# Optimization experiments

Hardware: AMD Instinct MI355X
Metric: run time of the kernel (lower is better)

## Reference

```python
import jax, jax.numpy as jnp
import numpy as np

DIM_IN = 32
DIM_OUT = 32
DIM_X = 64   # dim_internal
DIM_NL = 32
EPS_Q = 1e-4      # eps in default Q
TOL = 1e-3        # pos_def_tol
D22_EPS = 1.0     # d22_epsilon


def _model_param(X, Y, B2, C2, D12, D22_L, D22_U, D21, gamma):
    """Faithful port of REN_IQC_gamma._update_model_param (QR_fun=None, dim_in==dim_out)."""
    g = gamma[0, 0]
    Q = -EPS_Q * jnp.eye(DIM_OUT)
    R = -2.0 * g * jnp.eye(DIM_IN)
    S = jnp.eye(DIM_OUT, DIM_IN)
    # D22 = base + sym + skew (dim_in == dim_out)
    D22 = (g + D22_EPS) * jnp.eye(DIM_OUT, DIM_IN) + D22_L.T @ D22_L + (D22_U - D22_U.T)
    SD = S @ D22
    R_cal = R + SD + SD.T + D22.T @ Q @ D22
    R_cal_inv = jnp.linalg.inv(R_cal)
    M = D22.T @ Q + S
    C2_cal = M @ C2                      # (dim_in, dim_x)
    D21_cal = M @ D21 - D12.T            # (dim_in, dim_nl)
    vec_r = jnp.concatenate([C2_cal.T, D21_cal.T, B2], axis=0)   # (2*dim_x+dim_nl, dim_in)
    psi_r = vec_r @ R_cal_inv @ vec_r.T
    vec_q = jnp.concatenate([C2.T, D21.T, jnp.zeros((DIM_X, DIM_OUT), X.dtype)], axis=0)
    psi_q = vec_q @ Q @ vec_q.T
    n = 2 * DIM_X + DIM_NL
    H = X.T @ X + TOL * jnp.eye(n) + psi_r - psi_q
    i1, i2 = DIM_X, DIM_X + DIM_NL
    H11 = H[:i1, :i1]
    H21 = H[i1:i2, :i1]
    H22 = H[i1:i2, i1:i2]
    H31 = H[i2:, :i1]
    H32 = H[i2:, i1:i2]
    H33 = H[i2:, i2:]
    E = 0.5 * (H11 + H33 + Y - Y.T)
    E_inv = jnp.linalg.inv(E)
    Lam = 0.5 * jnp.diag(H22)            # Lambda (dim_nl,)
    D11 = -jnp.tril(H22, k=-1)           # strictly lower triangular
    C1 = -H21
    Fm = H31
    B1 = H32
    return Fm, B1, E_inv, Lam, D11, C1, D22


def reference(u_in, x0, X, Y, B2, C2, D12, D22_L, D22_U, D21, gamma):
    # Parameters are constant across time steps, so the per-step recompute in the
    # torch code collapses to a single evaluation with identical math.
    Fm, B1, E_inv, Lam, D11, C1, D22 = _model_param(X, Y, B2, C2, D12, D22_L, D22_U, D21, gamma)
    B = u_in.shape[0]
    nl_idx = jnp.arange(DIM_NL)

    def step(x, u_t):                    # x: (B, DIM_X), u_t: (B, DIM_IN)
        a = x @ C1.T + u_t @ D12.T       # (B, DIM_NL), constant part of v

        def inner(w, i):                 # forward substitution over strictly-lower D11
            v = a[:, i] + w @ D11[i]     # (B,)
            w = w.at[:, i].set(jnp.tanh(v / Lam[i]))
            return w, None

        w, _ = jax.lax.scan(inner, jnp.zeros((B, DIM_NL), u_in.dtype), nl_idx)
        x_new = (x @ Fm.T + w @ B1.T + u_t @ B2.T) @ E_inv.T
        y_t = x_new @ C2.T + w @ D21.T + u_t @ D22.T
        return x_new, y_t

    u_time = jnp.swapaxes(u_in, 0, 1)    # (T, B, DIM_IN)
    _, ys = jax.lax.scan(step, x0[:, 0, :], u_time)
    return jnp.swapaxes(ys, 0, 1)        # (B, T, DIM_OUT)


def setup_inputs() -> dict:
    key = jax.random.key(0)
    ks = jax.random.split(key, 10)
    std = 0.5
    n = 2 * DIM_X + DIM_NL
    B, T = 2048, 256
    return {
        "u_in": jax.random.normal(ks[0], (B, T, DIM_IN), jnp.float32),
        "x0": jax.random.normal(ks[1], (B, 1, DIM_X), jnp.float32),
        "X": jax.random.normal(ks[2], (n, n), jnp.float32) * std,
        "Y": jax.random.normal(ks[3], (DIM_X, DIM_X), jnp.float32) * std,
        "B2": jax.random.normal(ks[4], (DIM_X, DIM_IN), jnp.float32) * std,
        "C2": jax.random.normal(ks[5], (DIM_OUT, DIM_X), jnp.float32) * std,
        "D12": jax.random.normal(ks[6], (DIM_NL, DIM_IN), jnp.float32) * std,
        "D22_L": jax.random.normal(ks[7], (DIM_IN, DIM_IN), jnp.float32) * std,
        "D22_U": jax.random.normal(ks[8], (DIM_OUT, DIM_IN), jnp.float32) * std,
        "D21": jnp.zeros((DIM_OUT, DIM_NL), jnp.float32),   # registered buffer, fixed zero
        "gamma": jax.random.normal(ks[9], (1, 1), jnp.float32) * 3.0,
    }
```

## Files before the change

kernel.cpp:

```cpp
#include <hip/hip_runtime.h>
#include <math.h>

#define EPS_Q 1e-4
#define TOLC  1e-3

#define OFF_D22   0
#define OFF_RINV  1024
#define OFF_VR    2048
#define OFF_T1    7168
#define OFF_H     12288
#define OFF_E     37888
#define OFF_EI    41984
#define OFF_TMP   46080
#define OFF_TMP2  50176
#define D_END     54272

__global__ __launch_bounds__(256, 1) void prep1(
    const float* __restrict__ B2, const float* __restrict__ C2,
    const float* __restrict__ D12, const float* __restrict__ L,
    const float* __restrict__ U, const float* __restrict__ D21,
    const float* __restrict__ gam, double* __restrict__ wsd)
{
  __shared__ double aug[32][65];
  __shared__ double sFac[32];
  __shared__ int sPiv;
  const int tid = threadIdx.x;
  const double g = (double)gam[0];
  double* D22d = wsd + OFF_D22;

  for (int idx = tid; idx < 1024; idx += 256) {
    int i = idx >> 5, j = idx & 31;
    double s = (i == j) ? (g + 1.0) : 0.0;
    for (int k = 0; k < 32; ++k) s += (double)L[k*32+i] * (double)L[k*32+j];
    s += (double)U[i*32+j] - (double)U[j*32+i];
    D22d[idx] = s;
  }
  __syncthreads();
  for (int idx = tid; idx < 1024; idx += 256) {
    int i = idx >> 5, j = idx & 31;
    double s = (i == j) ? (-2.0 * g) : 0.0;
    s += D22d[i*32+j] + D22d[j*32+i];
    double q = 0.0;
    for (int k = 0; k < 32; ++k) q += D22d[k*32+i] * D22d[k*32+j];
    aug[i][j] = s - EPS_Q * q;
    aug[i][32+j] = (i == j) ? 1.0 : 0.0;
  }
  __syncthreads();
  for (int k = 0; k < 32; ++k) {
    if (tid < 64) {
      float mv = -1.f; int mi = k;
      if (tid < 32 && tid >= k) { mv = (float)fabs(aug[tid][k]); mi = tid; }
      #pragma unroll
      for (int o = 32; o; o >>= 1) {
        float ov = __shfl_xor(mv, o); int oi = __shfl_xor(mi, o);
        if (ov > mv) { mv = ov; mi = oi; }
      }
      if (tid == 0) sPiv = mi;
    }
    __syncthreads();
    int p = sPiv;
    if (p != k) for (int c = tid; c < 64; c += 256) { double t1 = aug[k][c]; aug[k][c] = aug[p][c]; aug[p][c] = t1; }
    __syncthreads();
    double pinv = 1.0 / aug[k][k];
    if (tid < 32 && tid != k) sFac[tid] = aug[tid][k];
    __syncthreads();
    for (int c = tid; c < 64; c += 256) aug[k][c] *= pinv;
    __syncthreads();
    for (int idx = tid; idx < 2048; idx += 256) {
      int r = idx >> 6, c = idx & 63;
      if (r != k) aug[r][c] -= sFac[r] * aug[k][c];
    }
    __syncthreads();
  }
  double* Rinv = wsd + OFF_RINV;
  for (int idx = tid; idx < 1024; idx += 256) Rinv[idx] = aug[idx >> 5][32 + (idx & 31)];

  double* vr = wsd + OFF_VR;
  for (int idx = tid; idx < 64*32; idx += 256) {
    int p = idx >> 5, k = idx & 31;
    double q = 0.0;
    for (int m = 0; m < 32; ++m) q += D22d[m*32+k] * (double)C2[m*64+p];
    vr[p*32+k] = (double)C2[k*64+p] - EPS_Q * q;
  }
  for (int idx = tid; idx < 32*32; idx += 256) {
    int p = idx >> 5, k = idx & 31;
    double q = 0.0;
    for (int m = 0; m < 32; ++m) q += D22d[m*32+k] * (double)D21[m*32+p];
    vr[(64+p)*32+k] = (double)D21[k*32+p] - EPS_Q * q - (double)D12[p*32+k];
  }
  for (int idx = tid; idx < 64*32; idx += 256) {
    int p = idx >> 5, k = idx & 31;
    vr[(96+p)*32+k] = (double)B2[p*32+k];
  }
  __syncthreads();
  double* T1 = wsd + OFF_T1;
  for (int idx = tid; idx < 160*32; idx += 256) {
    int p = idx >> 5, k2 = idx & 31;
    double s = 0.0;
    for (int k = 0; k < 32; ++k) s += vr[p*32+k] * Rinv[k*32+k2];
    T1[idx] = s;
  }
}

__global__ __launch_bounds__(256, 1) void prep2(
    const float* __restrict__ X, const float* __restrict__ C2,
    const float* __restrict__ D21, double* __restrict__ wsd)
{
  const double* vr = wsd + OFF_VR;
  const double* T1 = wsd + OFF_T1;
  double* H = wsd + OFF_H;
  int bi = blockIdx.x / 10, bj = blockIdx.x % 10;
  int i = bi*16 + (threadIdx.x >> 4);
  int j = bj*16 + (threadIdx.x & 15);
  double s = (i == j) ? TOLC : 0.0;
  for (int k = 0; k < 160; ++k) s += (double)X[k*160+i] * (double)X[k*160+j];
  double pr = 0.0;
  for (int k = 0; k < 32; ++k) pr += T1[i*32+k] * vr[j*32+k];
  s += pr;
  if (i < 96 && j < 96) {
    double vq = 0.0;
    for (int k = 0; k < 32; ++k) {
      double a = (i < 64) ? (double)C2[k*64+i] : (double)D21[k*32+(i-64)];
      double b = (j < 64) ? (double)C2[k*64+j] : (double)D21[k*32+(j-64)];
      vq += a*b;
    }
    s += EPS_Q * vq;
  }
  H[i*160+j] = s;
}

__global__ __launch_bounds__(256, 1) void prep3(
    const float* __restrict__ Y, const float* __restrict__ B2,
    const float* __restrict__ C2, const float* __restrict__ D12,
    const float* __restrict__ D21, double* __restrict__ wsd)
{
  __shared__ float aug[64][130];
  __shared__ float sFac[64];
  __shared__ int sPiv;
  const int tid = threadIdx.x;
  double* H   = wsd + OFF_H;
  double* Ed  = wsd + OFF_E;
  double* Ei  = wsd + OFF_EI;
  double* Tm  = wsd + OFF_TMP;
  double* Tm2 = wsd + OFF_TMP2;
  double* D22d = wsd + OFF_D22;
  float* fb = (float*)(wsd + D_END);

  for (int idx = tid; idx < 4096; idx += 256) {
    int i = idx >> 6, j = idx & 63;
    double e = 0.5*(H[i*160+j] + H[(96+i)*160+(96+j)] + (double)Y[i*64+j] - (double)Y[j*64+i]);
    Ed[idx] = e;
    aug[i][j] = (float)e;
    aug[i][64+j] = (i == j) ? 1.f : 0.f;
  }
  __syncthreads();
  for (int k = 0; k < 64; ++k) {
    if (tid < 64) {
      float mv = -1.f; int mi = k;
      if (tid >= k) { mv = fabsf(aug[tid][k]); mi = tid; }
      #pragma unroll
      for (int o = 32; o; o >>= 1) {
        float ov = __shfl_xor(mv, o); int oi = __shfl_xor(mi, o);
        if (ov > mv) { mv = ov; mi = oi; }
      }
      if (tid == 0) sPiv = mi;
    }
    __syncthreads();
    int p = sPiv;
    if (p != k) for (int c = tid; c < 128; c += 256) { float t1 = aug[k][c]; aug[k][c] = aug[p][c]; aug[p][c] = t1; }
    __syncthreads();
    float pinv = 1.0f / aug[k][k];
    if (tid < 64 && tid != k) sFac[tid] = aug[tid][k];
    __syncthreads();
    for (int c = tid; c < 128; c += 256) aug[k][c] *= pinv;
    __syncthreads();
    for (int idx = tid; idx < 64*128; idx += 256) {
      int r = idx >> 7, c = idx & 127;
      if (r != k) aug[r][c] -= sFac[r] * aug[k][c];
    }
    __syncthreads();
  }
  for (int idx = tid; idx < 4096; idx += 256) Ei[idx] = (double)aug[idx >> 6][64 + (idx & 63)];
  __syncthreads();
  for (int it = 0; it < 2; ++it) {
    for (int idx = tid; idx < 4096; idx += 256) {
      int i = idx >> 6, j = idx & 63;
      double s = (i == j) ? 2.0 : 0.0;
      for (int k = 0; k < 64; ++k) s -= Ed[i*64+k] * Ei[k*64+j];
      Tm[idx] = s;
    }
    __syncthreads();
    for (int idx = tid; idx < 4096; idx += 256) {
      int i = idx >> 6, j = idx & 63;
      double s = 0.0;
      for (int k = 0; k < 64; ++k) s += Ei[i*64+k] * Tm[k*64+j];
      Tm2[idx] = s;
    }
    __syncthreads();
    for (int idx = tid; idx < 4096; idx += 256) Ei[idx] = Tm2[idx];
    __syncthreads();
  }
  for (int idx = tid; idx < 64*128; idx += 256) {
    int r = idx >> 7, col = idx & 127;
    double s = 0.0;
    if (col < 64)       { for (int k = 0; k < 64; ++k) s += Ei[r*64+k] * H[(96+k)*160 + col]; }
    else if (col < 96)  { int jj = col-64; for (int k = 0; k < 64; ++k) s += Ei[r*64+k] * H[(96+k)*160 + 64 + jj]; }
    else                { int jj = col-96; for (int k = 0; k < 64; ++k) s += Ei[r*64+k] * (double)B2[k*32+jj]; }
    fb[((col >> 2)*64 + r)*4 + (col & 3)] = (float)s;
  }
  for (int idx = tid; idx < 32*128; idx += 256) {
    int r = idx >> 7, col = idx & 127;
    float v;
    if (col < 64)      v = C2[r*64 + col];
    else if (col < 96) v = D21[r*32 + (col-64)];
    else               v = (float)D22d[r*32 + (col-96)];
    fb[8192 + ((col >> 2)*32 + r)*4 + (col & 3)] = v;
  }
  for (int idx = tid; idx < 1024; idx += 256) {
    int i = idx >> 5, j = idx & 31;
    double li = 2.0 / H[(64+i)*160 + 64+i];
    fb[12288 + idx] = (j < i) ? (float)(-H[(64+i)*160 + 64+j] * li) : 0.f;
  }
  for (int idx = tid; idx < 32*96; idx += 256) {
    int r = idx / 96, j = idx % 96;
    double li = 2.0 / H[(64+r)*160 + 64+r];
    double v = (j < 64) ? (-H[(64+r)*160 + j] * li) : ((double)D12[r*32 + (j-64)] * li);
    fb[13312 + idx] = (float)v;
  }
}

__device__ __forceinline__ float frcp(float x) {
#if __has_builtin(__builtin_amdgcn_rcpf)
  return __builtin_amdgcn_rcpf(x);
#else
  return 1.0f / x;
#endif
}
__device__ __forceinline__ float ftanh(float x) {
  float xc = fminf(fmaxf(x, -15.f), 15.f);
  float E = __builtin_exp2f(xc * 2.8853900817779268f);
  return 1.f - 2.f * frcp(E + 1.f);
}
__device__ __forceinline__ float hsum4(float4 a) { return (a.x + a.y) + (a.z + a.w); }

__global__ __launch_bounds__(256, 2) void ren_main(
    const float* __restrict__ u_in, const float* __restrict__ x0,
    const double* __restrict__ wsd, float* __restrict__ out)
{
  __shared__ __align__(16) float sW[12288];
  __shared__ __align__(16) float sXU[4][132];
  const float* fb = (const float*)(wsd + D_END);
  const int tid = threadIdx.x;
  {
    const float4* g4 = (const float4*)fb;
    float4* s4 = (float4*)sW;
    for (int i = tid; i < 3072; i += 256) s4[i] = g4[i];
  }
  const int wv = tid >> 6, l = tid & 63;
  const int r = l & 31, lh = l >> 5;
  const int e = blockIdx.x * 4 + wv;
  float* xu = &sXU[wv][0];
  float4 wa[12];
  {
    const float4* WaG = (const float4*)(fb + 13312);
    #pragma unroll
    for (int c = 0; c < 12; ++c) wa[c] = WaG[r*24 + lh*12 + c];
  }
  float d11[32];
  {
    const float4* DG = (const float4*)(fb + 12288);
    #pragma unroll
    for (int c = 0; c < 8; ++c) {
      float4 dv = DG[r*8 + c];
      d11[4*c+0] = dv.x; d11[4*c+1] = dv.y; d11[4*c+2] = dv.z; d11[4*c+3] = dv.w;
    }
  }
  xu[l] = x0[(size_t)e*64 + l];
  xu[96 + r] = u_in[(size_t)e*8192 + r];
  __syncthreads();
  const float4* xu4  = (const float4*)xu;
  const float4* WxT4 = (const float4*)sW;
  const float4* WyT4 = (const float4*)(sW + 8192);
  const float* uG = u_in + (size_t)e * 8192;
  float* oG = out + (size_t)e * 8192;

  for (int t = 0; t < 256; ++t) {
    const int tn = (t < 255) ? (t + 1) : 255;
    float unext = uG[tn*32 + r];
    float4 s4 = make_float4(0.f, 0.f, 0.f, 0.f);
    #pragma unroll
    for (int c = 0; c < 12; ++c) {
      int ch = lh*12 + c;
      int xi = (ch < 16) ? ch : (ch + 8);
      float4 xv = xu4[xi]; float4 wv4 = wa[c];
      s4.x = fmaf(wv4.x, xv.x, s4.x); s4.y = fmaf(wv4.y, xv.y, s4.y);
      s4.z = fmaf(wv4.z, xv.z, s4.z); s4.w = fmaf(wv4.w, xv.w, s4.w);
    }
    float a = hsum4(s4);
    a += __shfl_xor(a, 32);
    float4 P4 = make_float4(0.f, 0.f, 0.f, 0.f);
    #pragma unroll
    for (int c = 0; c < 16; ++c) {
      float4 wv4 = WxT4[(c << 6) + l]; float4 xv = xu4[c];
      P4.x = fmaf(wv4.x, xv.x, P4.x); P4.y = fmaf(wv4.y, xv.y, P4.y);
      P4.z = fmaf(wv4.z, xv.z, P4.z); P4.w = fmaf(wv4.w, xv.w, P4.w);
    }
    #pragma unroll
    for (int c = 24; c < 32; ++c) {
      float4 wv4 = WxT4[(c << 6) + l]; float4 xv = xu4[c];
      P4.x = fmaf(wv4.x, xv.x, P4.x); P4.y = fmaf(wv4.y, xv.y, P4.y);
      P4.z = fmaf(wv4.z, xv.z, P4.z); P4.w = fmaf(wv4.w, xv.w, P4.w);
    }
    float4 Q4 = make_float4(0.f, 0.f, 0.f, 0.f);
    #pragma unroll
    for (int c = 0; c < 4; ++c) {
      int ch = 24 + lh*4 + c;
      float4 wv4 = WyT4[(ch << 5) + r]; float4 xv = xu4[ch];
      Q4.x = fmaf(wv4.x, xv.x, Q4.x); Q4.y = fmaf(wv4.y, xv.y, Q4.y);
      Q4.z = fmaf(wv4.z, xv.z, Q4.z); Q4.w = fmaf(wv4.w, xv.w, Q4.w);
    }
    float v = a;
    #pragma unroll
    for (int j = 0; j < 31; ++j) {
      float tt = ftanh(v);
      float b = __int_as_float(__builtin_amdgcn_readlane(__float_as_int(tt), j));
      v = fmaf(d11[j], b, v);
    }
    float myw = ftanh(v);
    xu[64 + r] = myw;
    #pragma unroll
    for (int c = 16; c < 24; ++c) {
      float4 wv4 = WxT4[(c << 6) + l]; float4 xv = xu4[c];
      P4.x = fmaf(wv4.x, xv.x, P4.x); P4.y = fmaf(wv4.y, xv.y, P4.y);
      P4.z = fmaf(wv4.z, xv.z, P4.z); P4.w = fmaf(wv4.w, xv.w, P4.w);
    }
    xu[l] = hsum4(P4);
    #pragma unroll
    for (int c = 0; c < 12; ++c) {
      int ch = lh*12 + c;
      float4 wv4 = WyT4[(ch << 5) + r]; float4 xv = xu4[ch];
      Q4.x = fmaf(wv4.x, xv.x, Q4.x); Q4.y = fmaf(wv4.y, xv.y, Q4.y);
      Q4.z = fmaf(wv4.z, xv.z, Q4.z); Q4.w = fmaf(wv4.w, xv.w, Q4.w);
    }
    float y = hsum4(Q4);
    y += __shfl_xor(y, 32);
    if (l < 32) oG[t*32 + l] = y;
    xu[96 + r] = unext;
  }
}

extern "C" void kernel_launch(void* const* d_in, const int* in_sizes, int n_in,
                              void* d_out, int out_size, void* d_ws, size_t ws_size,
                              hipStream_t stream)
{
  const float* u_in = (const float*)d_in[0];
  const float* x0   = (const float*)d_in[1];
  const float* X    = (const float*)d_in[2];
  const float* Y    = (const float*)d_in[3];
  const float* B2   = (const float*)d_in[4];
  const float* C2   = (const float*)d_in[5];
  const float* D12  = (const float*)d_in[6];
  const float* L    = (const float*)d_in[7];
  const float* U    = (const float*)d_in[8];
  const float* D21  = (const float*)d_in[9];
  const float* gam  = (const float*)d_in[10];
  double* wsd = (double*)d_ws;
  float* out = (float*)d_out;

  hipLaunchKernelGGL(prep1, dim3(1), dim3(256), 0, stream, B2, C2, D12, L, U, D21, gam, wsd);
  hipLaunchKernelGGL(prep2, dim3(100), dim3(256), 0, stream, X, C2, D21, wsd);
  hipLaunchKernelGGL(prep3, dim3(1), dim3(256), 0, stream, Y, B2, C2, D12, D21, wsd);
  hipLaunchKernelGGL(ren_main, dim3(512), dim3(256), 0, stream, u_in, x0, wsd, out);
}
```

Measured before the change: 1.533 ms.

## Map one batch element per half-wave and interleave tanh chain with matvec

Each 32-lane half-wave now handles its own batch element, so a wave runs two elements and the grid is halved. This removes the cross-half shuffles for the nonlinearity input and the output. The tanh scaling constant is folded into the precomputed D11 and input weights, which drops the clamp and multiply from each tanh. The serial 31-step forward-substitution chain now broadcasts with ds_swizzle inside the half-wave and is interleaved with the independent state and output matvec chunks, so those FMAs can hide the chain's latency. In exchange, per-thread register pressure is much higher (24 float4 weights plus two 32-entry arrays), occupancy drops to one block per CU, and the removed clamp relies on exp2 overflow to infinity behaving correctly.

```diff
diff --git a/kernel.cpp b/kernel.cpp
--- a/kernel.cpp
+++ b/kernel.cpp
@@ -145,6 +145,7 @@
   double* Tm2 = wsd + OFF_TMP2;
   double* D22d = wsd + OFF_D22;
   float* fb = (float*)(wsd + D_END);
+  const double KS = 2.8853900817779268;
 
   for (int idx = tid; idx < 4096; idx += 256) {
     int i = idx >> 6, j = idx & 63;
@@ -219,13 +220,14 @@
   for (int idx = tid; idx < 1024; idx += 256) {
     int i = idx >> 5, j = idx & 31;
     double li = 2.0 / H[(64+i)*160 + 64+i];
-    fb[12288 + idx] = (j < i) ? (float)(-H[(64+i)*160 + 64+j] * li) : 0.f;
-  }
+    fb[12288 + idx] = (j < i) ? (float)(-H[(64+i)*160 + 64+j] * li * KS) : 0.f;
+  }
+  for (int idx = tid; idx < 32*96; ++idx, idx += 255) {}
   for (int idx = tid; idx < 32*96; idx += 256) {
     int r = idx / 96, j = idx % 96;
     double li = 2.0 / H[(64+r)*160 + 64+r];
     double v = (j < 64) ? (-H[(64+r)*160 + j] * li) : ((double)D12[r*32 + (j-64)] * li);
-    fb[13312 + idx] = (float)v;
+    fb[13312 + idx] = (float)(v * KS);
   }
 }
 
@@ -236,19 +238,14 @@
   return 1.0f / x;
 #endif
 }
-__device__ __forceinline__ float ftanh(float x) {
-  float xc = fminf(fmaxf(x, -15.f), 15.f);
-  float E = __builtin_exp2f(xc * 2.8853900817779268f);
-  return 1.f - 2.f * frcp(E + 1.f);
-}
 __device__ __forceinline__ float hsum4(float4 a) { return (a.x + a.y) + (a.z + a.w); }
 
-__global__ __launch_bounds__(256, 2) void ren_main(
+__global__ __launch_bounds__(256, 1) void ren_main(
     const float* __restrict__ u_in, const float* __restrict__ x0,
     const double* __restrict__ wsd, float* __restrict__ out)
 {
   __shared__ __align__(16) float sW[12288];
-  __shared__ __align__(16) float sXU[4][132];
+  __shared__ __align__(16) float sXU[4][2][132];
   const float* fb = (const float*)(wsd + D_END);
   const int tid = threadIdx.x;
   {
@@ -257,16 +254,17 @@
     for (int i = tid; i < 3072; i += 256) s4[i] = g4[i];
   }
   const int wv = tid >> 6, l = tid & 63;
-  const int r = l & 31, lh = l >> 5;
-  const int e = blockIdx.x * 4 + wv;
-  float* xu = &sXU[wv][0];
-  float4 wa[12];
+  const int sub = l >> 5, r = l & 31;
+  const int e = blockIdx.x * 8 + wv * 2 + sub;
+  float* xu = &sXU[wv][sub][0];
+
+  float4 wa[24];
   {
     const float4* WaG = (const float4*)(fb + 13312);
     #pragma unroll
-    for (int c = 0; c < 12; ++c) wa[c] = WaG[r*24 + lh*12 + c];
-  }
-  float d11[32];
+    for (int c = 0; c < 24; ++c) wa[c] = WaG[r*24 + c];
+  }
+  float d11[32], m2d[32];
   {
     const float4* DG = (const float4*)(fb + 12288);
     #pragma unroll
@@ -274,10 +272,14 @@
       float4 dv = DG[r*8 + c];
       d11[4*c+0] = dv.x; d11[4*c+1] = dv.y; d11[4*c+2] = dv.z; d11[4*c+3] = dv.w;
     }
-  }
-  xu[l] = x0[(size_t)e*64 + l];
+    #pragma unroll
+    for (int j = 0; j < 32; ++j) m2d[j] = -2.f * d11[j];
+  }
+  xu[r]      = x0[(size_t)e*64 + r];
+  xu[32 + r] = x0[(size_t)e*64 + 32 + r];
   xu[96 + r] = u_in[(size_t)e*8192 + r];
   __syncthreads();
+
   const float4* xu4  = (const float4*)xu;
   const float4* WxT4 = (const float4*)sW;
   const float4* WyT4 = (const float4*)(sW + 8192);
@@ -287,65 +289,97 @@
   for (int t = 0; t < 256; ++t) {
     const int tn = (t < 255) ? (t + 1) : 255;
     float unext = uG[tn*32 + r];
-    float4 s4 = make_float4(0.f, 0.f, 0.f, 0.f);
+    float4 sA0 = make_float4(0.f,0.f,0.f,0.f), sA1 = make_float4(0.f,0.f,0.f,0.f);
     #pragma unroll
-    for (int c = 0; c < 12; ++c) {
-      int ch = lh*12 + c;
-      int xi = (ch < 16) ? ch : (ch + 8);
-      float4 xv = xu4[xi]; float4 wv4 = wa[c];
-      s4.x = fmaf(wv4.x, xv.x, s4.x); s4.y = fmaf(wv4.y, xv.y, s4.y);
-      s4.z = fmaf(wv4.z, xv.z, s4.z); s4.w = fmaf(wv4.w, xv.w, s4.w);
-    }
-    float a = hsum4(s4);
-    a += __shfl_xor(a, 32);
-    float4 P4 = make_float4(0.f, 0.f, 0.f, 0.f);
+    for (int c = 0; c < 24; c += 2) {
+      int xi0 = (c   < 16) ? c     : (c + 8);
+      int xi1 = (c+1 < 16) ? (c+1) : (c + 9);
+      float4 xv0 = xu4[xi0]; float4 xv1 = xu4[xi1];
+      sA0.x = fmaf(wa[c].x, xv0.x, sA0.x);   sA0.y = fmaf(wa[c].y, xv0.y, sA0.y);
+      sA0.z = fmaf(wa[c].z, xv0.z, sA0.z);   sA0.w = fmaf(wa[c].w, xv0.w, sA0.w);
+      sA1.x = fmaf(wa[c+1].x, xv1.x, sA1.x); sA1.y = fmaf(wa[c+1].y, xv1.y, sA1.y);
+      sA1.z = fmaf(wa[c+1].z, xv1.z, sA1.z); sA1.w = fmaf(wa[c+1].w, xv1.w, sA1.w);
+    }
+    float v = hsum4(sA0) + hsum4(sA1);
+
+    float4 P0 = make_float4(0.f,0.f,0.f,0.f);
+    float4 P1 = make_float4(0.f,0.f,0.f,0.f);
+    float4 Q  = make_float4(0.f,0.f,0.f,0.f);
+
+#define XCHUNK(c) { float4 xv = xu4[c]; \
+      float4 w0 = WxT4[((c) << 6) + r]; float4 w1 = WxT4[((c) << 6) + 32 + r]; \
+      P0.x = fmaf(w0.x, xv.x, P0.x); P0.y = fmaf(w0.y, xv.y, P0.y); \
+      P0.z = fmaf(w0.z, xv.z, P0.z); P0.w = fmaf(w0.w, xv.w, P0.w); \
+      P1.x = fmaf(w1.x, xv.x, P1.x); P1.y = fmaf(w1.y, xv.y, P1.y); \
+      P1.z = fmaf(w1.z, xv.z, P1.z); P1.w = fmaf(w1.w, xv.w, P1.w); }
+#define XYCHUNK(c) { float4 xv = xu4[c]; \
+      float4 w0 = WxT4[((c) << 6) + r]; float4 w1 = WxT4[((c) << 6) + 32 + r]; \
+      float4 wy = WyT4[((c) << 5) + r]; \
+      P0.x = fmaf(w0.x, xv.x, P0.x); P0.y = fmaf(w0.y, xv.y, P0.y); \
+      P0.z = fmaf(w0.z, xv.z, P0.z); P0.w = fmaf(w0.w, xv.w, P0.w); \
+      P1.x = fmaf(w1.x, xv.x, P1.x); P1.y = fmaf(w1.y, xv.y, P1.y); \
+      P1.z = fmaf(w1.z, xv.z, P1.z); P1.w = fmaf(w1.w, xv.w, P1.w); \
+      Q.x  = fmaf(wy.x, xv.x, Q.x);  Q.y  = fmaf(wy.y, xv.y, Q.y); \
+      Q.z  = fmaf(wy.z, xv.z, Q.z);  Q.w  = fmaf(wy.w, xv.w, Q.w); }
+#define CPRE(j) float E_##j = __builtin_exp2f(v); \
+      float rr_##j = frcp(E_##j + 1.f); \
+      float br_##j = __int_as_float(__builtin_amdgcn_ds_swizzle(__float_as_int(rr_##j), ((j) << 5)));
+#define CPOST(j) v = fmaf(m2d[j], br_##j, v + d11[j]);
+
+    CPRE(0)  XCHUNK(0)   CPOST(0)
+    CPRE(1)  XCHUNK(1)   CPOST(1)
+    CPRE(2)  XCHUNK(2)   CPOST(2)
+    CPRE(3)  XCHUNK(3)   CPOST(3)
+    CPRE(4)  XCHUNK(4)   CPOST(4)
+    CPRE(5)  XCHUNK(5)   CPOST(5)
+    CPRE(6)  XCHUNK(6)   CPOST(6)
+    CPRE(7)  XCHUNK(7)   CPOST(7)
+    CPRE(8)  XCHUNK(8)   CPOST(8)
+    CPRE(9)  XCHUNK(9)   CPOST(9)
+    CPRE(10) XCHUNK(10)  CPOST(10)
+    CPRE(11) XCHUNK(11)  CPOST(11)
+    CPRE(12) XCHUNK(12)  CPOST(12)
+    CPRE(13) XCHUNK(13)  CPOST(13)
+    CPRE(14) XCHUNK(14)  CPOST(14)
+    CPRE(15) XCHUNK(15)  CPOST(15)
+    CPRE(16) XYCHUNK(24) CPOST(16)
+    CPRE(17) XYCHUNK(25) CPOST(17)
+    CPRE(18) XYCHUNK(26) CPOST(18)
+    CPRE(19) XYCHUNK(27) CPOST(19)
+    CPRE(20) XYCHUNK(28) CPOST(20)
+    CPRE(21) XYCHUNK(29) CPOST(21)
+    CPRE(22) XYCHUNK(30) CPOST(22)
+    CPRE(23) XYCHUNK(31) CPOST(23)
+    CPRE(24) CPOST(24)
+    CPRE(25) CPOST(25)
+    CPRE(26) CPOST(26)
+    CPRE(27) CPOST(27)
+    CPRE(28) CPOST(28)
+    CPRE(29) CPOST(29)
+    CPRE(30) CPOST(30)
+
+    float Ef = __builtin_exp2f(v);
+    float myw = 1.f - 2.f * frcp(Ef + 1.f);
+    xu[64 + r] = myw;
+    XYCHUNK(16) XYCHUNK(17) XYCHUNK(18) XYCHUNK(19)
+    XYCHUNK(20) XYCHUNK(21) XYCHUNK(22) XYCHUNK(23)
+    xu[r]      = hsum4(P0);
+    xu[32 + r] = hsum4(P1);
     #pragma unroll
     for (int c = 0; c < 16; ++c) {
-      float4 wv4 = WxT4[(c << 6) + l]; float4 xv = xu4[c];
-      P4.x = fmaf(wv4.x, xv.x, P4.x); P4.y = fmaf(wv4.y, xv.y, P4.y);
-      P4.z = fmaf(wv4.z, xv.z, P4.z); P4.w = fmaf(wv4.w, xv.w, P4.w);
-    }
-    #pragma unroll
-    for (int c = 24; c < 32; ++c) {
-      float4 wv4 = WxT4[(c << 6) + l]; float4 xv = xu4[c];
-      P4.x = fmaf(wv4.x, xv.x, P4.x); P4.y = fmaf(wv4.y, xv.y, P4.y);
-      P4.z = fmaf(wv4.z, xv.z, P4.z); P4.w = fmaf(wv4.w, xv.w, P4.w);
-    }
-    float4 Q4 = make_float4(0.f, 0.f, 0.f, 0.f);
-    #pragma unroll
-    for (int c = 0; c < 4; ++c) {
-      int ch = 24 + lh*4 + c;
-      float4 wv4 = WyT4[(ch << 5) + r]; float4 xv = xu4[ch];
-      Q4.x = fmaf(wv4.x, xv.x, Q4.x); Q4.y = fmaf(wv4.y, xv.y, Q4.y);
-      Q4.z = fmaf(wv4.z, xv.z, Q4.z); Q4.w = fmaf(wv4.w, xv.w, Q4.w);
-    }
-    float v = a;
-    #pragma unroll
-    for (int j = 0; j < 31; ++j) {
-      float tt = ftanh(v);
-      float b = __int_as_float(__builtin_amdgcn_readlane(__float_as_int(tt), j));
-      v = fmaf(d11[j], b, v);
-    }
-    float myw = ftanh(v);
-    xu[64 + r] = myw;
-    #pragma unroll
-    for (int c = 16; c < 24; ++c) {
-      float4 wv4 = WxT4[(c << 6) + l]; float4 xv = xu4[c];
-      P4.x = fmaf(wv4.x, xv.x, P4.x); P4.y = fmaf(wv4.y, xv.y, P4.y);
-      P4.z = fmaf(wv4.z, xv.z, P4.z); P4.w = fmaf(wv4.w, xv.w, P4.w);
-    }
-    xu[l] = hsum4(P4);
-    #pragma unroll
-    for (int c = 0; c < 12; ++c) {
-      int ch = lh*12 + c;
-      float4 wv4 = WyT4[(ch << 5) + r]; float4 xv = xu4[ch];
-      Q4.x = fmaf(wv4.x, xv.x, Q4.x); Q4.y = fmaf(wv4.y, xv.y, Q4.y);
-      Q4.z = fmaf(wv4.z, xv.z, Q4.z); Q4.w = fmaf(wv4.w, xv.w, Q4.w);
-    }
-    float y = hsum4(Q4);
-    y += __shfl_xor(y, 32);
-    if (l < 32) oG[t*32 + l] = y;
+      float4 xv = xu4[c];
+      float4 wy = WyT4[(c << 5) + r];
+      Q.x = fmaf(wy.x, xv.x, Q.x); Q.y = fmaf(wy.y, xv.y, Q.y);
+      Q.z = fmaf(wy.z, xv.z, Q.z); Q.w = fmaf(wy.w, xv.w, Q.w);
+    }
+    float y = hsum4(Q);
+    oG[t*32 + r] = y;
     xu[96 + r] = unext;
+
+#undef XCHUNK
+#undef XYCHUNK
+#undef CPRE
+#undef CPOST
   }
 }
 
@@ -370,5 +404,5 @@
   hipLaunchKernelGGL(prep1, dim3(1), dim3(256), 0, stream, B2, C2, D12, L, U, D21, gam, wsd);
   hipLaunchKernelGGL(prep2, dim3(100), dim3(256), 0, stream, X, C2, D21, wsd);
   hipLaunchKernelGGL(prep3, dim3(1), dim3(256), 0, stream, Y, B2, C2, D12, D21, wsd);
-  hipLaunchKernelGGL(ren_main, dim3(512), dim3(256), 0, stream, u_in, x0, wsd, out);
-}
+  hipLaunchKernelGGL(ren_main, dim3(256), dim3(256), 0, stream, u_in, x0, wsd, out);
+}
```

Result: slower. 1.727 ms (+12.6%).

## Hold Wx weights in registers, prescale tanh constants, widen prep3 block

Applied to the files above, without the earlier changes.

The main kernel now keeps the 64x128 state-update weight slice in per-lane registers and stages only the output and nonlinearity-input weights in shared memory, with the latter transposed for conflict-free access. The tanh scaling constant is folded into the D11 and input weights during prep, which removes a multiply and the clamp from the serial forward-substitution chain. prep3 runs with 1024 threads so its Gauss-Jordan and Newton refinement steps finish in fewer passes. Dropping the clamp risks exp overflow for large pre-activations, and the 128 extra VGPRs per lane may cause spills or lower occupancy.

```diff
diff --git a/kernel.cpp b/kernel.cpp
--- a/kernel.cpp
+++ b/kernel.cpp
@@ -129,7 +129,7 @@
   H[i*160+j] = s;
 }
 
-__global__ __launch_bounds__(256, 1) void prep3(
+__global__ __launch_bounds__(1024, 1) void prep3(
     const float* __restrict__ Y, const float* __restrict__ B2,
     const float* __restrict__ C2, const float* __restrict__ D12,
     const float* __restrict__ D21, double* __restrict__ wsd)
@@ -145,8 +145,9 @@
   double* Tm2 = wsd + OFF_TMP2;
   double* D22d = wsd + OFF_D22;
   float* fb = (float*)(wsd + D_END);
-
-  for (int idx = tid; idx < 4096; idx += 256) {
+  const double KS = 2.8853900817779268;
+
+  for (int idx = tid; idx < 4096; idx += 1024) {
     int i = idx >> 6, j = idx & 63;
     double e = 0.5*(H[i*160+j] + H[(96+i)*160+(96+j)] + (double)Y[i*64+j] - (double)Y[j*64+i]);
     Ed[idx] = e;
@@ -167,40 +168,40 @@
     }
     __syncthreads();
     int p = sPiv;
-    if (p != k) for (int c = tid; c < 128; c += 256) { float t1 = aug[k][c]; aug[k][c] = aug[p][c]; aug[p][c] = t1; }
+    if (p != k) for (int c = tid; c < 128; c += 1024) { float t1 = aug[k][c]; aug[k][c] = aug[p][c]; aug[p][c] = t1; }
     __syncthreads();
     float pinv = 1.0f / aug[k][k];
     if (tid < 64 && tid != k) sFac[tid] = aug[tid][k];
     __syncthreads();
-    for (int c = tid; c < 128; c += 256) aug[k][c] *= pinv;
-    __syncthreads();
-    for (int idx = tid; idx < 64*128; idx += 256) {
+    for (int c = tid; c < 128; c += 1024) aug[k][c] *= pinv;
+    __syncthreads();
+    for (int idx = tid; idx < 64*128; idx += 1024) {
       int r = idx >> 7, c = idx & 127;
       if (r != k) aug[r][c] -= sFac[r] * aug[k][c];
     }
     __syncthreads();
   }
-  for (int idx = tid; idx < 4096; idx += 256) Ei[idx] = (double)aug[idx >> 6][64 + (idx & 63)];
+  for (int idx = tid; idx < 4096; idx += 1024) Ei[idx] = (double)aug[idx >> 6][64 + (idx & 63)];
   __syncthreads();
   for (int it = 0; it < 2; ++it) {
-    for (int idx = tid; idx < 4096; idx += 256) {
+    for (int idx = tid; idx < 4096; idx += 1024) {
       int i = idx >> 6, j = idx & 63;
       double s = (i == j) ? 2.0 : 0.0;
       for (int k = 0; k < 64; ++k) s -= Ed[i*64+k] * Ei[k*64+j];
       Tm[idx] = s;
     }
     __syncthreads();
-    for (int idx = tid; idx < 4096; idx += 256) {
+    for (int idx = tid; idx < 4096; idx += 1024) {
       int i = idx >> 6, j = idx & 63;
       double s = 0.0;
       for (int k = 0; k < 64; ++k) s += Ei[i*64+k] * Tm[k*64+j];
       Tm2[idx] = s;
     }
     __syncthreads();
-    for (int idx = tid; idx < 4096; idx += 256) Ei[idx] = Tm2[idx];
-    __syncthreads();
-  }
-  for (int idx = tid; idx < 64*128; idx += 256) {
+    for (int idx = tid; idx < 4096; idx += 1024) Ei[idx] = Tm2[idx];
+    __syncthreads();
+  }
+  for (int idx = tid; idx < 64*128; idx += 1024) {
     int r = idx >> 7, col = idx & 127;
     double s = 0.0;
     if (col < 64)       { for (int k = 0; k < 64; ++k) s += Ei[r*64+k] * H[(96+k)*160 + col]; }
@@ -208,7 +209,7 @@
     else                { int jj = col-96; for (int k = 0; k < 64; ++k) s += Ei[r*64+k] * (double)B2[k*32+jj]; }
     fb[((col >> 2)*64 + r)*4 + (col & 3)] = (float)s;
   }
-  for (int idx = tid; idx < 32*128; idx += 256) {
+  for (int idx = tid; idx < 32*128; idx += 1024) {
     int r = idx >> 7, col = idx & 127;
     float v;
     if (col < 64)      v = C2[r*64 + col];
@@ -216,16 +217,16 @@
     else               v = (float)D22d[r*32 + (col-96)];
     fb[8192 + ((col >> 2)*32 + r)*4 + (col & 3)] = v;
   }
-  for (int idx = tid; idx < 1024; idx += 256) {
+  for (int idx = tid; idx < 1024; idx += 1024) {
     int i = idx >> 5, j = idx & 31;
     double li = 2.0 / H[(64+i)*160 + 64+i];
-    fb[12288 + idx] = (j < i) ? (float)(-H[(64+i)*160 + 64+j] * li) : 0.f;
-  }
-  for (int idx = tid; idx < 32*96; idx += 256) {
+    fb[12288 + idx] = (j < i) ? (float)(-H[(64+i)*160 + 64+j] * li * KS) : 0.f;
+  }
+  for (int idx = tid; idx < 32*96; idx += 1024) {
     int r = idx / 96, j = idx % 96;
     double li = 2.0 / H[(64+r)*160 + 64+r];
     double v = (j < 64) ? (-H[(64+r)*160 + j] * li) : ((double)D12[r*32 + (j-64)] * li);
-    fb[13312 + idx] = (float)v;
+    fb[13312 + idx] = (float)(v * KS);
   }
 }
 
@@ -236,35 +237,35 @@
   return 1.0f / x;
 #endif
 }
-__device__ __forceinline__ float ftanh(float x) {
-  float xc = fminf(fmaxf(x, -15.f), 15.f);
-  float E = __builtin_exp2f(xc * 2.8853900817779268f);
-  return 1.f - 2.f * frcp(E + 1.f);
-}
 __device__ __forceinline__ float hsum4(float4 a) { return (a.x + a.y) + (a.z + a.w); }
 
 __global__ __launch_bounds__(256, 2) void ren_main(
     const float* __restrict__ u_in, const float* __restrict__ x0,
     const double* __restrict__ wsd, float* __restrict__ out)
 {
-  __shared__ __align__(16) float sW[12288];
+  __shared__ __align__(16) float sW[7168];
   __shared__ __align__(16) float sXU[4][132];
   const float* fb = (const float*)(wsd + D_END);
   const int tid = threadIdx.x;
   {
     const float4* g4 = (const float4*)fb;
     float4* s4 = (float4*)sW;
-    for (int i = tid; i < 3072; i += 256) s4[i] = g4[i];
+    for (int i = tid; i < 1024; i += 256) s4[i] = g4[2048 + i];
+    for (int i = tid; i < 768; i += 256) {
+      int r2 = i / 24, ch = i % 24;
+      s4[1024 + ch*32 + r2] = g4[3328 + i];
+    }
   }
   const int wv = tid >> 6, l = tid & 63;
   const int r = l & 31, lh = l >> 5;
   const int e = blockIdx.x * 4 + wv;
   float* xu = &sXU[wv][0];
-  float4 wa[12];
+
+  float4 wx[32];
   {
-    const float4* WaG = (const float4*)(fb + 13312);
-    #pragma unroll
-    for (int c = 0; c < 12; ++c) wa[c] = WaG[r*24 + lh*12 + c];
+    const float4* WxG = (const float4*)fb;
+    #pragma unroll
+    for (int c = 0; c < 32; ++c) wx[c] = WxG[(c << 6) + l];
   }
   float d11[32];
   {
@@ -278,75 +279,68 @@
   xu[l] = x0[(size_t)e*64 + l];
   xu[96 + r] = u_in[(size_t)e*8192 + r];
   __syncthreads();
+
   const float4* xu4  = (const float4*)xu;
-  const float4* WxT4 = (const float4*)sW;
-  const float4* WyT4 = (const float4*)(sW + 8192);
+  const float4* WyT4 = (const float4*)sW;
+  const float4* WaT4 = (const float4*)sW + 1024;
   const float* uG = u_in + (size_t)e * 8192;
   float* oG = out + (size_t)e * 8192;
+
+#define FMA4(A, W, XV) \
+  A.x = fmaf(W.x, XV.x, A.x); A.y = fmaf(W.y, XV.y, A.y); \
+  A.z = fmaf(W.z, XV.z, A.z); A.w = fmaf(W.w, XV.w, A.w);
 
   for (int t = 0; t < 256; ++t) {
     const int tn = (t < 255) ? (t + 1) : 255;
     float unext = uG[tn*32 + r];
-    float4 s4 = make_float4(0.f, 0.f, 0.f, 0.f);
+    float4 sA = make_float4(0.f, 0.f, 0.f, 0.f);
     #pragma unroll
     for (int c = 0; c < 12; ++c) {
       int ch = lh*12 + c;
       int xi = (ch < 16) ? ch : (ch + 8);
-      float4 xv = xu4[xi]; float4 wv4 = wa[c];
-      s4.x = fmaf(wv4.x, xv.x, s4.x); s4.y = fmaf(wv4.y, xv.y, s4.y);
-      s4.z = fmaf(wv4.z, xv.z, s4.z); s4.w = fmaf(wv4.w, xv.w, s4.w);
-    }
-    float a = hsum4(s4);
+      float4 xv = xu4[xi]; float4 wv4 = WaT4[ch*32 + r];
+      FMA4(sA, wv4, xv)
+    }
+    float a = hsum4(sA);
     a += __shfl_xor(a, 32);
     float4 P4 = make_float4(0.f, 0.f, 0.f, 0.f);
     #pragma unroll
-    for (int c = 0; c < 16; ++c) {
-      float4 wv4 = WxT4[(c << 6) + l]; float4 xv = xu4[c];
-      P4.x = fmaf(wv4.x, xv.x, P4.x); P4.y = fmaf(wv4.y, xv.y, P4.y);
-      P4.z = fmaf(wv4.z, xv.z, P4.z); P4.w = fmaf(wv4.w, xv.w, P4.w);
-    }
-    #pragma unroll
-    for (int c = 24; c < 32; ++c) {
-      float4 wv4 = WxT4[(c << 6) + l]; float4 xv = xu4[c];
-      P4.x = fmaf(wv4.x, xv.x, P4.x); P4.y = fmaf(wv4.y, xv.y, P4.y);
-      P4.z = fmaf(wv4.z, xv.z, P4.z); P4.w = fmaf(wv4.w, xv.w, P4.w);
-    }
+    for (int c = 0; c < 16; ++c) { float4 xv = xu4[c]; FMA4(P4, wx[c], xv) }
+    #pragma unroll
+    for (int c = 24; c < 32; ++c) { float4 xv = xu4[c]; FMA4(P4, wx[c], xv) }
     float4 Q4 = make_float4(0.f, 0.f, 0.f, 0.f);
     #pragma unroll
     for (int c = 0; c < 4; ++c) {
       int ch = 24 + lh*4 + c;
-      float4 wv4 = WyT4[(ch << 5) + r]; float4 xv = xu4[ch];
-      Q4.x = fmaf(wv4.x, xv.x, Q4.x); Q4.y = fmaf(wv4.y, xv.y, Q4.y);
-      Q4.z = fmaf(wv4.z, xv.z, Q4.z); Q4.w = fmaf(wv4.w, xv.w, Q4.w);
+      float4 xv = xu4[ch]; float4 wv4 = WyT4[(ch << 5) + r];
+      FMA4(Q4, wv4, xv)
     }
     float v = a;
     #pragma unroll
     for (int j = 0; j < 31; ++j) {
-      float tt = ftanh(v);
-      float b = __int_as_float(__builtin_amdgcn_readlane(__float_as_int(tt), j));
+      float E = __builtin_exp2f(v);
+      float w = fmaf(-2.f, frcp(E + 1.f), 1.f);
+      float b = __int_as_float(__builtin_amdgcn_readlane(__float_as_int(w), j));
       v = fmaf(d11[j], b, v);
     }
-    float myw = ftanh(v);
+    float Ef = __builtin_exp2f(v);
+    float myw = fmaf(-2.f, frcp(Ef + 1.f), 1.f);
     xu[64 + r] = myw;
     #pragma unroll
-    for (int c = 16; c < 24; ++c) {
-      float4 wv4 = WxT4[(c << 6) + l]; float4 xv = xu4[c];
-      P4.x = fmaf(wv4.x, xv.x, P4.x); P4.y = fmaf(wv4.y, xv.y, P4.y);
-      P4.z = fmaf(wv4.z, xv.z, P4.z); P4.w = fmaf(wv4.w, xv.w, P4.w);
-    }
+    for (int c = 16; c < 24; ++c) { float4 xv = xu4[c]; FMA4(P4, wx[c], xv) }
     xu[l] = hsum4(P4);
     #pragma unroll
     for (int c = 0; c < 12; ++c) {
       int ch = lh*12 + c;
-      float4 wv4 = WyT4[(ch << 5) + r]; float4 xv = xu4[ch];
-      Q4.x = fmaf(wv4.x, xv.x, Q4.x); Q4.y = fmaf(wv4.y, xv.y, Q4.y);
-      Q4.z = fmaf(wv4.z, xv.z, Q4.z); Q4.w = fmaf(wv4.w, xv.w, Q4.w);
+      float4 xv = xu4[ch]; float4 wv4 = WyT4[(ch << 5) + r];
+      FMA4(Q4, wv4, xv)
     }
     float y = hsum4(Q4);
     y += __shfl_xor(y, 32);
     if (l < 32) oG[t*32 + l] = y;
     xu[96 + r] = unext;
   }
+#undef FMA4
 }
 
 extern "C" void kernel_launch(void* const* d_in, const int* in_sizes, int n_in,
@@ -369,6 +363,6 @@
 
   hipLaunchKernelGGL(prep1, dim3(1), dim3(256), 0, stream, B2, C2, D12, L, U, D21, gam, wsd);
   hipLaunchKernelGGL(prep2, dim3(100), dim3(256), 0, stream, X, C2, D21, wsd);
-  hipLaunchKernelGGL(prep3, dim3(1), dim3(256), 0, stream, Y, B2, C2, D12, D21, wsd);
+  hipLaunchKernelGGL(prep3, dim3(1), dim3(1024), 0, stream, Y, B2, C2, D12, D21, wsd);
   hipLaunchKernelGGL(ren_main, dim3(512), dim3(256), 0, stream, u_in, x0, wsd, out);
 }
```

Result: slower. 1.675 ms (+9.3%).
